# Performance work log

Hardware: AMD Instinct MI355X
Metric: run time of the kernel (lower is better)

The kernel has to match this reference:

```python
import jax, jax.numpy as jnp
import numpy as np

H, C = 4, 32            # heads, per-head out channels
N, E = 25000, 400000    # nodes, edges
NODE_DIM, EDGE_DIM = 256, 64
HC = H * C
IN_DIMS = [NODE_DIM, NODE_DIM + HC, NODE_DIM + HC]


def _conv(h, src, dst, ea, Wq, bq, Wk, bk, Wv, bv, We, Ws, bs):
    """One PyG-style TransformerConv (concat=True, root_weight=True, beta=False)."""
    n = h.shape[0]
    q = (h @ Wq + bq).reshape(n, H, C)
    k = (h @ Wk + bk).reshape(n, H, C)
    v = (h @ Wv + bv).reshape(n, H, C)
    e = (ea @ We).reshape(-1, H, C)            # lin_edge has no bias in PyG
    kj = k[src] + e                             # (E,H,C) key + edge feature
    alpha = jnp.einsum('ehc,ehc->eh', q[dst], kj) / jnp.asarray(np.sqrt(C), h.dtype)
    # segment softmax over incoming edges of each destination node
    amax = jax.ops.segment_max(alpha, dst, num_segments=n)
    ex = jnp.exp(alpha - amax[dst])
    denom = jax.ops.segment_sum(ex, dst, num_segments=n)
    a = ex / (denom[dst] + 1e-16)
    msg = (v[src] + e) * a[:, :, None]          # (E,H,C)
    out = jax.ops.segment_sum(msg, dst, num_segments=n).reshape(n, HC)
    return out + h @ Ws + bs                    # root/skip connection


def setup_inputs() -> dict:
    key = jax.random.key(0)
    ks = iter(jax.random.split(key, 64))
    inp = {}
    inp['x'] = jax.random.normal(next(ks), (N, NODE_DIM), dtype=jnp.float32)
    inp['edge_index'] = jax.random.randint(next(ks), (2, E), 0, N, dtype=jnp.int64)
    inp['edge_attr'] = jax.random.normal(next(ks), (E, EDGE_DIM), dtype=jnp.float32)
    s = 0.05
    for i, din in enumerate(IN_DIMS):
        inp[f'Wq{i}'] = jax.random.normal(next(ks), (din, HC), dtype=jnp.float32) * s
        inp[f'bq{i}'] = jnp.zeros((HC,), jnp.float32)
        inp[f'Wk{i}'] = jax.random.normal(next(ks), (din, HC), dtype=jnp.float32) * s
        inp[f'bk{i}'] = jnp.zeros((HC,), jnp.float32)
        inp[f'Wv{i}'] = jax.random.normal(next(ks), (din, HC), dtype=jnp.float32) * s
        inp[f'bv{i}'] = jnp.zeros((HC,), jnp.float32)
        inp[f'We{i}'] = jax.random.normal(next(ks), (EDGE_DIM, HC), dtype=jnp.float32) * s
        inp[f'Ws{i}'] = jax.random.normal(next(ks), (din, HC), dtype=jnp.float32) * s
        inp[f'bs{i}'] = jnp.zeros((HC,), jnp.float32)
    inp['Wout'] = jax.random.normal(next(ks), (HC, C), dtype=jnp.float32) * s
    inp['bout'] = jnp.zeros((C,), jnp.float32)
    return inp


def reference(x, edge_index, edge_attr,
              Wq0, bq0, Wk0, bk0, Wv0, bv0, We0, Ws0, bs0,
              Wq1, bq1, Wk1, bk1, Wv1, bv1, We1, Ws1, bs1,
              Wq2, bq2, Wk2, bk2, Wv2, bv2, We2, Ws2, bs2,
              Wout, bout):
    src, dst = edge_index[0], edge_index[1]
    params = [
        (Wq0, bq0, Wk0, bk0, Wv0, bv0, We0, Ws0, bs0),
        (Wq1, bq1, Wk1, bk1, Wv1, bv1, We1, Ws1, bs1),
        (Wq2, bq2, Wk2, bk2, Wv2, bv2, We2, Ws2, bs2),
    ]
    h = _conv(x, src, dst, edge_attr, *params[0])
    for p in params[1:]:
        h = _conv(jnp.concatenate([h, x], axis=-1), src, dst, edge_attr, *p)
    return h @ Wout + bout  # (N, output_dim)
```

## Files before the change

kernel.cpp:

```cpp
#include <hip/hip_runtime.h>
#include <hip/hip_bf16.h>
#include <math.h>

#define HCX 128
#define EDX 64
#define KPAD 384

typedef short bf16x8 __attribute__((ext_vector_type(8)));
typedef float f32x4  __attribute__((ext_vector_type(4)));

__device__ __forceinline__ short f2bf(float v) {
    __hip_bfloat16 b = __float2bfloat16(v);
    return *reinterpret_cast<short*>(&b);
}
__device__ __forceinline__ float bf2f(short s) {
    __hip_bfloat16 b = *reinterpret_cast<__hip_bfloat16*>(&s);
    return __bfloat162float(b);
}
__device__ __forceinline__ void gload16(const short* g, short* l) {
    __builtin_amdgcn_global_load_lds((const __attribute__((address_space(1))) void*)g,
                                     (__attribute__((address_space(3))) void*)l, 16, 0, 0);
}

__global__ __launch_bounds__(256) void k_zero_deg(int* __restrict__ deg, int n) {
    int t = blockIdx.x * 256 + threadIdx.x;
    if (t < n) deg[t] = 0;
}

__global__ __launch_bounds__(256) void k_hist(const int* __restrict__ dst, int* __restrict__ deg, int nE) {
    int t = blockIdx.x * 256 + threadIdx.x;
    if (t < nE) atomicAdd(&deg[dst[t]], 1);
}

__global__ __launch_bounds__(1024) void k_scan(const int* __restrict__ deg, int* __restrict__ csr_off,
                                               int* __restrict__ cursor, int nN) {
    __shared__ int sums[1024];
    int t = threadIdx.x;
    int chunk = (nN + 1023) >> 10;
    int lo = min(t * chunk, nN), hi = min(lo + chunk, nN);
    int s = 0;
    for (int i = lo; i < hi; ++i) s += deg[i];
    sums[t] = s;
    __syncthreads();
    for (int off = 1; off < 1024; off <<= 1) {
        int v = (t >= off) ? sums[t - off] : 0;
        __syncthreads();
        sums[t] += v;
        __syncthreads();
    }
    int run = (t == 0) ? 0 : sums[t - 1];
    for (int i = lo; i < hi; ++i) {
        csr_off[i] = run; cursor[i] = run;
        run += deg[i];
    }
    if (t == 1023) csr_off[nN] = sums[1023];
}

__global__ __launch_bounds__(256) void k_scatter(const int* __restrict__ dst, const int* __restrict__ src,
                                                 int* __restrict__ cursor,
                                                 int* __restrict__ edge_sorted, int* __restrict__ src_sorted,
                                                 int nE) {
    int t = blockIdx.x * 256 + threadIdx.x;
    if (t < nE) {
        int pos = atomicAdd(&cursor[dst[t]], 1);
        edge_sorted[pos] = t;
        src_sorted[pos]  = src[t];
    }
}

__global__ __launch_bounds__(256) void k_cvt_h(const float* __restrict__ pH, int has_h,
                                               short* __restrict__ Ah, short* __restrict__ Al,
                                               int nN, int Mpad)
{
    int t = blockIdx.x * 256 + threadIdx.x;
    int row = t >> 5;
    if (row >= Mpad) return;
    int c0 = (t & 31) * 4;
    float4 v = make_float4(0.f, 0.f, 0.f, 0.f);
    if (has_h && row < nN) v = *(const float4*)(pH + (size_t)row * HCX + c0);
    short4 hs, ls;
    hs.x = f2bf(v.x); ls.x = f2bf(v.x - bf2f(hs.x));
    hs.y = f2bf(v.y); ls.y = f2bf(v.y - bf2f(hs.y));
    hs.z = f2bf(v.z); ls.z = f2bf(v.z - bf2f(hs.z));
    hs.w = f2bf(v.w); ls.w = f2bf(v.w - bf2f(hs.w));
    *(short4*)(Ah + (size_t)row * KPAD + c0) = hs;
    *(short4*)(Al + (size_t)row * KPAD + c0) = ls;
}

__global__ __launch_bounds__(256) void k_cvt_x(const float* __restrict__ x,
                                               short* __restrict__ Ah, short* __restrict__ Al,
                                               int nN, int Mpad)
{
    int t = blockIdx.x * 256 + threadIdx.x;
    int row = t >> 6;
    if (row >= Mpad) return;
    int c0 = (t & 63) * 4;
    float4 v = make_float4(0.f, 0.f, 0.f, 0.f);
    if (row < nN) v = *(const float4*)(x + (size_t)row * 256 + c0);
    short4 hs, ls;
    hs.x = f2bf(v.x); ls.x = f2bf(v.x - bf2f(hs.x));
    hs.y = f2bf(v.y); ls.y = f2bf(v.y - bf2f(hs.y));
    hs.z = f2bf(v.z); ls.z = f2bf(v.z - bf2f(hs.z));
    hs.w = f2bf(v.w); ls.w = f2bf(v.w - bf2f(hs.w));
    *(short4*)(Ah + (size_t)row * KPAD + 128 + c0) = hs;
    *(short4*)(Al + (size_t)row * KPAD + 128 + c0) = ls;
}

__global__ __launch_bounds__(384) void k_cvt_W(const float* __restrict__ Wq, const float* __restrict__ Wk,
                                               const float* __restrict__ Wv, const float* __restrict__ Ws,
                                               int koff, int dinW,
                                               short* __restrict__ Wth, short* __restrict__ Wtl)
{
    int col = blockIdx.x;
    int g = col >> 7, c = col & 127;
    const float* W = (g == 0) ? Wq : (g == 1) ? Wk : (g == 2) ? Wv : Ws;
    for (int k = threadIdx.x; k < KPAD; k += blockDim.x) {
        int kr = k - koff;
        float v = (kr >= 0 && kr < dinW) ? W[(size_t)kr * HCX + c] : 0.f;
        short h = f2bf(v);
        Wth[(size_t)col * KPAD + k] = h;
        Wtl[(size_t)col * KPAD + k] = f2bf(v - bf2f(h));
    }
}

__global__ __launch_bounds__(256) void k_gemm(
    const short* __restrict__ Ah, const short* __restrict__ Al,
    const short* __restrict__ Wth, const short* __restrict__ Wtl,
    const float* __restrict__ bq, const float* __restrict__ bk,
    const float* __restrict__ bv, const float* __restrict__ bs,
    float* __restrict__ qkvs, int nN)
{
    __shared__ short AsH[128 * 32];
    __shared__ short AsL[128 * 32];
    __shared__ short BsH[128 * 32];
    __shared__ short BsL[128 * 32];

    const int rowB = blockIdx.x * 128;
    const int g = blockIdx.y;
    const int colB = g * 128;
    const int tid = threadIdx.x;
    const int w = tid >> 6, l = tid & 63;

    f32x4 acc[4][4];
    #pragma unroll
    for (int i = 0; i < 4; ++i)
        #pragma unroll
        for (int j = 0; j < 4; ++j)
            acc[i][j] = (f32x4){0.f, 0.f, 0.f, 0.f};

    const int lrow4 = l >> 2;
    const int gch = (l & 3) ^ ((l >> 3) & 3);
    const int lr = l & 15, kg = l >> 4;

    for (int ks = 0; ks < KPAD / 32; ++ks) {
        const int k0 = ks * 32;
        #pragma unroll
        for (int jj = 0; jj < 2; ++jj) {
            int j = w + jj * 4;
            int rr = j * 16 + lrow4;
            size_t aoff = (size_t)(rowB + rr) * KPAD + k0 + gch * 8;
            size_t boff = (size_t)(colB + rr) * KPAD + k0 + gch * 8;
            gload16(Ah  + aoff, AsH + j * 512);
            gload16(Al  + aoff, AsL + j * 512);
            gload16(Wth + boff, BsH + j * 512);
            gload16(Wtl + boff, BsL + j * 512);
        }
        __syncthreads();

        bf16x8 ah[4], am[4], bh[4], bm[4];
        #pragma unroll
        for (int mi = 0; mi < 4; ++mi) {
            int r = (w >> 1) * 64 + mi * 16 + lr;
            int ch = kg ^ ((r >> 1) & 3);
            int off = r * 32 + ch * 8;
            ah[mi] = *(const bf16x8*)(AsH + off);
            am[mi] = *(const bf16x8*)(AsL + off);
        }
        #pragma unroll
        for (int ni = 0; ni < 4; ++ni) {
            int c = (w & 1) * 64 + ni * 16 + lr;
            int ch = kg ^ ((c >> 1) & 3);
            int off = c * 32 + ch * 8;
            bh[ni] = *(const bf16x8*)(BsH + off);
            bm[ni] = *(const bf16x8*)(BsL + off);
        }
        #pragma unroll
        for (int mi = 0; mi < 4; ++mi)
            #pragma unroll
            for (int ni = 0; ni < 4; ++ni) {
                acc[mi][ni] = __builtin_amdgcn_mfma_f32_16x16x32_bf16(ah[mi], bh[ni], acc[mi][ni], 0, 0, 0);
                acc[mi][ni] = __builtin_amdgcn_mfma_f32_16x16x32_bf16(ah[mi], bm[ni], acc[mi][ni], 0, 0, 0);
                acc[mi][ni] = __builtin_amdgcn_mfma_f32_16x16x32_bf16(am[mi], bh[ni], acc[mi][ni], 0, 0, 0);
            }
        __syncthreads();
    }

    const float* bias = (g == 0) ? bq : (g == 1) ? bk : (g == 2) ? bv : bs;
    float* outp = qkvs + (size_t)g * nN * HCX;
    const int lq = l >> 4;
    #pragma unroll
    for (int mi = 0; mi < 4; ++mi)
        #pragma unroll
        for (int ni = 0; ni < 4; ++ni) {
            int c = (w & 1) * 64 + ni * 16 + lr;
            float bb = bias[c];
            #pragma unroll
            for (int j = 0; j < 4; ++j) {
                int r = rowB + (w >> 1) * 64 + mi * 16 + lq * 4 + j;
                if (r < nN) outp[(size_t)r * HCX + c] = acc[mi][ni][j] + bb;
            }
        }
}

__global__ __launch_bounds__(256) void k_qwe(const float* __restrict__ qpl,
                                             const float* __restrict__ We,
                                             float* __restrict__ qWe, int nN)
{
    __shared__ float Wes[64 * 128];
    __shared__ float qs[16][128];
    for (int i = threadIdx.x; i < 64 * 128; i += 256) {
        int d = i >> 7, c = i & 127;
        Wes[d * 128 + ((c + d) & 127)] = We[i];
    }
    int nb = blockIdx.x * 16;
    for (int i = threadIdx.x; i < 16 * 128; i += 256) {
        int r = i >> 7, c = i & 127;
        int row = nb + r;
        qs[r][c] = (row < nN) ? qpl[(size_t)row * HCX + c] : 0.f;
    }
    __syncthreads();
    int h = threadIdx.x >> 6, d = threadIdx.x & 63;
    const int base = h * 32;
    for (int r = 0; r < 16; ++r) {
        int row = nb + r;
        if (row >= nN) break;
        float s = 0.f;
        #pragma unroll
        for (int c = 0; c < 32; ++c)
            s += qs[r][base + c] * Wes[d * 128 + ((base + c + d) & 127)];
        qWe[(size_t)row * 256 + threadIdx.x] = s;
    }
}

__global__ __launch_bounds__(256) void k_edge(
    const float* __restrict__ qkvs, const float* __restrict__ qWe,
    const float* __restrict__ ea,   const float* __restrict__ We,
    const int* __restrict__ csr_off, const int* __restrict__ edge_sorted,
    const int* __restrict__ src_sorted,
    float* __restrict__ hout, int nN)
{
    __shared__ float wea_s[4][4][64];
    const int wv = threadIdx.x >> 6, l = threadIdx.x & 63;
    const int n = blockIdx.x * 4 + wv;
    const bool active = n < nN;
    int o0 = 0, o1 = 0;
    if (active) { o0 = csr_off[n]; o1 = csr_off[n + 1]; }

    const float* qpl = qkvs;
    const float* kpl = qkvs + (size_t)nN * HCX;
    const float* vpl = qkvs + 2 * (size_t)nN * HCX;

    float qr0 = 0.f, qr1 = 0.f, qw0 = 0.f, qw1 = 0.f, qw2 = 0.f, qw3 = 0.f;
    if (active) {
        qr0 = qpl[(size_t)n * HCX + l];
        qr1 = qpl[(size_t)n * HCX + 64 + l];
        const float* qw = qWe + (size_t)n * 256;
        qw0 = qw[l]; qw1 = qw[64 + l]; qw2 = qw[128 + l]; qw3 = qw[192 + l];
    }
    const int hsel = l >> 5;
    const float scale = 0.17677669529663687f;

    float m0 = -INFINITY, m1 = -INFINITY, m2 = -INFINITY, m3 = -INFINITY;
    float den0 = 0.f, den1 = 0.f, den2 = 0.f, den3 = 0.f;
    float w0 = 0.f, w1 = 0.f, w2 = 0.f, w3 = 0.f;
    float macc0 = 0.f, macc1 = 0.f;

    for (int i = o0; i < o1; ++i) {
        int eid = edge_sorted[i];
        int sn  = src_sorted[i];
        float kv0 = kpl[(size_t)sn * HCX + l];
        float kv1 = kpl[(size_t)sn * HCX + 64 + l];
        float vv0 = vpl[(size_t)sn * HCX + l];
        float vv1 = vpl[(size_t)sn * HCX + 64 + l];
        float eav = ea[(size_t)eid * EDX + l];

        float p1 = qr0 * kv0, p2 = qr1 * kv1;
        #pragma unroll
        for (int s = 1; s < 32; s <<= 1) {
            p1 += __shfl_xor(p1, s);
            p2 += __shfl_xor(p2, s);
        }
        float p1o = __shfl_xor(p1, 32), p2o = __shfl_xor(p2, 32);
        float qk0 = hsel ? p1o : p1, qk1 = hsel ? p1 : p1o;
        float qk2 = hsel ? p2o : p2, qk3 = hsel ? p2 : p2o;

        float t0 = eav * qw0, t1 = eav * qw1, t2 = eav * qw2, t3 = eav * qw3;
        #pragma unroll
        for (int s = 1; s < 64; s <<= 1) {
            t0 += __shfl_xor(t0, s); t1 += __shfl_xor(t1, s);
            t2 += __shfl_xor(t2, s); t3 += __shfl_xor(t3, s);
        }

        float s0 = (qk0 + t0) * scale, s1 = (qk1 + t1) * scale;
        float s2 = (qk2 + t2) * scale, s3 = (qk3 + t3) * scale;

        float nm0 = fmaxf(m0, s0), nm1 = fmaxf(m1, s1);
        float nm2 = fmaxf(m2, s2), nm3 = fmaxf(m3, s3);
        float f0 = __expf(m0 - nm0), f1 = __expf(m1 - nm1);
        float f2 = __expf(m2 - nm2), f3 = __expf(m3 - nm3);
        float e0 = __expf(s0 - nm0), e1 = __expf(s1 - nm1);
        float e2 = __expf(s2 - nm2), e3 = __expf(s3 - nm3);
        m0 = nm0; m1 = nm1; m2 = nm2; m3 = nm3;
        den0 = den0 * f0 + e0; den1 = den1 * f1 + e1;
        den2 = den2 * f2 + e2; den3 = den3 * f3 + e3;
        w0 = w0 * f0 + e0 * eav; w1 = w1 * f1 + e1 * eav;
        w2 = w2 * f2 + e2 * eav; w3 = w3 * f3 + e3 * eav;
        float fA = hsel ? f1 : f0, eA = hsel ? e1 : e0;
        float fB = hsel ? f3 : f2, eB = hsel ? e3 : e2;
        macc0 = macc0 * fA + eA * vv0;
        macc1 = macc1 * fB + eB * vv1;
    }

    wea_s[wv][0][l] = w0; wea_s[wv][1][l] = w1;
    wea_s[wv][2][l] = w2; wea_s[wv][3][l] = w3;
    __syncthreads();

    float acc1 = macc0, acc2 = macc1;
    const int h1 = hsel, h2 = 2 + hsel;
    #pragma unroll 8
    for (int d = 0; d < 64; ++d) {
        acc1 += wea_s[wv][h1][d] * We[d * HCX + l];
        acc2 += wea_s[wv][h2][d] * We[d * HCX + 64 + l];
    }
    if (active) {
        float d1 = (hsel ? den1 : den0) + 1e-16f;
        float d2 = (hsel ? den3 : den2) + 1e-16f;
        const float* spl = qkvs + 3 * (size_t)nN * HCX + (size_t)n * HCX;
        hout[(size_t)n * HCX + l]      = acc1 / d1 + spl[l];
        hout[(size_t)n * HCX + 64 + l] = acc2 / d2 + spl[64 + l];
    }
}

__global__ __launch_bounds__(256) void k_out(const float* __restrict__ h,
                                             const float* __restrict__ Wout,
                                             const float* __restrict__ bout,
                                             float* __restrict__ out, int nN)
{
    __shared__ float hs[8][128];
    int nb = blockIdx.x * 8;
    for (int i = threadIdx.x; i < 8 * 128; i += 256) {
        int r = i >> 7, c = i & 127;
        int row = nb + r;
        hs[r][c] = (row < nN) ? h[(size_t)row * 128 + c] : 0.f;
    }
    __syncthreads();
    int r = threadIdx.x >> 5, col = threadIdx.x & 31;
    int row = nb + r;
    if (row < nN) {
        float s = bout[col];
        #pragma unroll 16
        for (int c = 0; c < 128; ++c) s += hs[r][c] * Wout[c * 32 + col];
        out[(size_t)row * 32 + col] = s;
    }
}

static inline size_t align_up(size_t v, size_t a) { return (v + a - 1) & ~(a - 1); }

extern "C" void kernel_launch(void* const* d_in, const int* in_sizes, int n_in,
                              void* d_out, int out_size, void* d_ws, size_t ws_size,
                              hipStream_t stream)
{
    const float* x  = (const float*)d_in[0];
    const int*   ei = (const int*)d_in[1];
    const float* ea = (const float*)d_in[2];
    const int nN = in_sizes[0] / 256;
    const int nE = in_sizes[1] / 2;
    const int Mpad = (nN + 127) & ~127;
    const int* src = ei;
    const int* dst = ei + nE;

    char* p = (char*)d_ws;
    size_t off = 0;
    auto take = [&](size_t bytes) { void* r = p + off; off = align_up(off + bytes, 256); return r; };
    int* csr_off     = (int*)take((size_t)(nN + 1) * 4);
    int* cursor      = (int*)take((size_t)nN * 4);
    int* deg         = (int*)take((size_t)nN * 4);
    int* edge_sorted = (int*)take((size_t)nE * 4);
    int* src_sorted  = (int*)take((size_t)nE * 4);
    float* qkvs = (float*)take((size_t)4 * nN * HCX * 4);
    float* qWe  = (float*)take((size_t)nN * 256 * 4);
    float* h0   = (float*)take((size_t)nN * HCX * 4);
    float* h1   = (float*)take((size_t)nN * HCX * 4);
    short* Ah   = (short*)take((size_t)Mpad * KPAD * 2);
    short* Al   = (short*)take((size_t)Mpad * KPAD * 2);
    short* Wth  = (short*)take((size_t)512 * KPAD * 2);
    short* Wtl  = (short*)take((size_t)512 * KPAD * 2);
    (void)ws_size; (void)n_in; (void)out_size;

    k_zero_deg<<<(nN + 255) / 256, 256, 0, stream>>>(deg, nN);
    k_hist<<<(nE + 255) / 256, 256, 0, stream>>>(dst, deg, nE);
    k_scan<<<1, 1024, 0, stream>>>(deg, csr_off, cursor, nN);
    k_scatter<<<(nE + 255) / 256, 256, 0, stream>>>(dst, src, cursor, edge_sorted, src_sorted, nE);

    k_cvt_x<<<(Mpad * 64 + 255) / 256, 256, 0, stream>>>(x, Ah, Al, nN, Mpad);

    auto layer = [&](const float* pH, int has_h, int base, float* hout) {
        const float* Wq = (const float*)d_in[base + 0];
        const float* bq = (const float*)d_in[base + 1];
        const float* Wk = (const float*)d_in[base + 2];
        const float* bk = (const float*)d_in[base + 3];
        const float* Wv = (const float*)d_in[base + 4];
        const float* bv = (const float*)d_in[base + 5];
        const float* We = (const float*)d_in[base + 6];
        const float* Ws = (const float*)d_in[base + 7];
        const float* bs = (const float*)d_in[base + 8];
        int koff = has_h ? 0 : 128;
        int dinW = has_h ? 384 : 256;
        k_cvt_h<<<(Mpad * 32 + 255) / 256, 256, 0, stream>>>(pH, has_h, Ah, Al, nN, Mpad);
        k_cvt_W<<<512, 384, 0, stream>>>(Wq, Wk, Wv, Ws, koff, dinW, Wth, Wtl);
        dim3 gg(Mpad / 128, 4);
        k_gemm<<<gg, 256, 0, stream>>>(Ah, Al, Wth, Wtl, bq, bk, bv, bs, qkvs, nN);
        k_qwe<<<(nN + 15) / 16, 256, 0, stream>>>(qkvs, We, qWe, nN);
        k_edge<<<(nN + 3) / 4, 256, 0, stream>>>(qkvs, qWe, ea, We,
                                                 csr_off, edge_sorted, src_sorted, hout, nN);
    };

    layer(nullptr, 0, 3,  h0);
    layer(h0, 1,   12, h1);
    layer(h1, 1,   21, h0);

    k_out<<<(nN + 7) / 8, 256, 0, stream>>>(h0, (const float*)d_in[30], (const float*)d_in[31],
                                            (float*)d_out, nN);
}
```

Measured before the change: 1.130 ms.

## Split edge attention into per-edge score kernel and per-node aggregation

Moves the attention score computation into a separate edge-parallel kernel that writes exp(score) per edge and head, so the per-node aggregation loop no longer does shuffle reductions or online-softmax rescaling. A dst_sorted array is added so each edge thread can find its destination's query. The max subtraction is dropped, so exp can overflow for large scores, and the extra expA buffer adds global memory traffic.

Measured after the change: 1.134 ms. No clear change (+0.4%).

```diff
diff --git a/kernel.cpp b/kernel.cpp
--- a/kernel.cpp
+++ b/kernel.cpp
@@ -59,12 +59,14 @@
 __global__ __launch_bounds__(256) void k_scatter(const int* __restrict__ dst, const int* __restrict__ src,
                                                  int* __restrict__ cursor,
                                                  int* __restrict__ edge_sorted, int* __restrict__ src_sorted,
-                                                 int nE) {
+                                                 int* __restrict__ dst_sorted, int nE) {
     int t = blockIdx.x * 256 + threadIdx.x;
     if (t < nE) {
-        int pos = atomicAdd(&cursor[dst[t]], 1);
+        int d = dst[t];
+        int pos = atomicAdd(&cursor[d], 1);
         edge_sorted[pos] = t;
         src_sorted[pos]  = src[t];
+        dst_sorted[pos]  = d;
     }
 }
 
@@ -242,8 +244,41 @@
     }
 }
 
-__global__ __launch_bounds__(256) void k_edge(
+__global__ __launch_bounds__(256) void k_alpha(
     const float* __restrict__ qkvs, const float* __restrict__ qWe,
+    const float* __restrict__ ea,
+    const int* __restrict__ edge_sorted, const int* __restrict__ src_sorted,
+    const int* __restrict__ dst_sorted,
+    float* __restrict__ expA, int nN, int nE)
+{
+    int t = blockIdx.x * 256 + threadIdx.x;
+    int i = t >> 2, h = t & 3;
+    if (i >= nE) return;
+    int sn = src_sorted[i], dn = dst_sorted[i];
+    int eid = edge_sorted[i];
+
+    const float* q = qkvs + (size_t)dn * HCX + h * 32;
+    const float* k = qkvs + (size_t)nN * HCX + (size_t)sn * HCX + h * 32;
+    float s = 0.f;
+    #pragma unroll
+    for (int c = 0; c < 32; c += 4) {
+        float4 qv = *(const float4*)(q + c);
+        float4 kv = *(const float4*)(k + c);
+        s += qv.x * kv.x + qv.y * kv.y + qv.z * kv.z + qv.w * kv.w;
+    }
+    const float* qw = qWe + (size_t)dn * 256 + h * 64;
+    const float* ev = ea + (size_t)eid * EDX;
+    #pragma unroll
+    for (int d = 0; d < EDX; d += 4) {
+        float4 av = *(const float4*)(ev + d);
+        float4 wv = *(const float4*)(qw + d);
+        s += av.x * wv.x + av.y * wv.y + av.z * wv.z + av.w * wv.w;
+    }
+    expA[t] = __expf(s * 0.17677669529663687f);
+}
+
+__global__ __launch_bounds__(256) void k_edge2(
+    const float* __restrict__ qkvs, const float* __restrict__ expA,
     const float* __restrict__ ea,   const float* __restrict__ We,
     const int* __restrict__ csr_off, const int* __restrict__ edge_sorted,
     const int* __restrict__ src_sorted,
@@ -256,69 +291,28 @@
     int o0 = 0, o1 = 0;
     if (active) { o0 = csr_off[n]; o1 = csr_off[n + 1]; }
 
-    const float* qpl = qkvs;
-    const float* kpl = qkvs + (size_t)nN * HCX;
     const float* vpl = qkvs + 2 * (size_t)nN * HCX;
-
-    float qr0 = 0.f, qr1 = 0.f, qw0 = 0.f, qw1 = 0.f, qw2 = 0.f, qw3 = 0.f;
-    if (active) {
-        qr0 = qpl[(size_t)n * HCX + l];
-        qr1 = qpl[(size_t)n * HCX + 64 + l];
-        const float* qw = qWe + (size_t)n * 256;
-        qw0 = qw[l]; qw1 = qw[64 + l]; qw2 = qw[128 + l]; qw3 = qw[192 + l];
-    }
     const int hsel = l >> 5;
-    const float scale = 0.17677669529663687f;
-
-    float m0 = -INFINITY, m1 = -INFINITY, m2 = -INFINITY, m3 = -INFINITY;
+
     float den0 = 0.f, den1 = 0.f, den2 = 0.f, den3 = 0.f;
     float w0 = 0.f, w1 = 0.f, w2 = 0.f, w3 = 0.f;
     float macc0 = 0.f, macc1 = 0.f;
 
+    #pragma unroll 2
     for (int i = o0; i < o1; ++i) {
+        float4 e4 = *(const float4*)(expA + (size_t)i * 4);
         int eid = edge_sorted[i];
         int sn  = src_sorted[i];
-        float kv0 = kpl[(size_t)sn * HCX + l];
-        float kv1 = kpl[(size_t)sn * HCX + 64 + l];
+        float eav = ea[(size_t)eid * EDX + l];
         float vv0 = vpl[(size_t)sn * HCX + l];
         float vv1 = vpl[(size_t)sn * HCX + 64 + l];
-        float eav = ea[(size_t)eid * EDX + l];
-
-        float p1 = qr0 * kv0, p2 = qr1 * kv1;
-        #pragma unroll
-        for (int s = 1; s < 32; s <<= 1) {
-            p1 += __shfl_xor(p1, s);
-            p2 += __shfl_xor(p2, s);
-        }
-        float p1o = __shfl_xor(p1, 32), p2o = __shfl_xor(p2, 32);
-        float qk0 = hsel ? p1o : p1, qk1 = hsel ? p1 : p1o;
-        float qk2 = hsel ? p2o : p2, qk3 = hsel ? p2 : p2o;
-
-        float t0 = eav * qw0, t1 = eav * qw1, t2 = eav * qw2, t3 = eav * qw3;
-        #pragma unroll
-        for (int s = 1; s < 64; s <<= 1) {
-            t0 += __shfl_xor(t0, s); t1 += __shfl_xor(t1, s);
-            t2 += __shfl_xor(t2, s); t3 += __shfl_xor(t3, s);
-        }
-
-        float s0 = (qk0 + t0) * scale, s1 = (qk1 + t1) * scale;
-        float s2 = (qk2 + t2) * scale, s3 = (qk3 + t3) * scale;
-
-        float nm0 = fmaxf(m0, s0), nm1 = fmaxf(m1, s1);
-        float nm2 = fmaxf(m2, s2), nm3 = fmaxf(m3, s3);
-        float f0 = __expf(m0 - nm0), f1 = __expf(m1 - nm1);
-        float f2 = __expf(m2 - nm2), f3 = __expf(m3 - nm3);
-        float e0 = __expf(s0 - nm0), e1 = __expf(s1 - nm1);
-        float e2 = __expf(s2 - nm2), e3 = __expf(s3 - nm3);
-        m0 = nm0; m1 = nm1; m2 = nm2; m3 = nm3;
-        den0 = den0 * f0 + e0; den1 = den1 * f1 + e1;
-        den2 = den2 * f2 + e2; den3 = den3 * f3 + e3;
-        w0 = w0 * f0 + e0 * eav; w1 = w1 * f1 + e1 * eav;
-        w2 = w2 * f2 + e2 * eav; w3 = w3 * f3 + e3 * eav;
-        float fA = hsel ? f1 : f0, eA = hsel ? e1 : e0;
-        float fB = hsel ? f3 : f2, eB = hsel ? e3 : e2;
-        macc0 = macc0 * fA + eA * vv0;
-        macc1 = macc1 * fB + eB * vv1;
+
+        den0 += e4.x; den1 += e4.y; den2 += e4.z; den3 += e4.w;
+        w0 += e4.x * eav; w1 += e4.y * eav; w2 += e4.z * eav; w3 += e4.w * eav;
+        float eA = hsel ? e4.y : e4.x;
+        float eB = hsel ? e4.w : e4.z;
+        macc0 += eA * vv0;
+        macc1 += eB * vv1;
     }
 
     wea_s[wv][0][l] = w0; wea_s[wv][1][l] = w1;
@@ -387,8 +381,10 @@
     int* deg         = (int*)take((size_t)nN * 4);
     int* edge_sorted = (int*)take((size_t)nE * 4);
     int* src_sorted  = (int*)take((size_t)nE * 4);
+    int* dst_sorted  = (int*)take((size_t)nE * 4);
     float* qkvs = (float*)take((size_t)4 * nN * HCX * 4);
     float* qWe  = (float*)take((size_t)nN * 256 * 4);
+    float* expA = (float*)take((size_t)nE * 4 * 4);
     float* h0   = (float*)take((size_t)nN * HCX * 4);
     float* h1   = (float*)take((size_t)nN * HCX * 4);
     short* Ah   = (short*)take((size_t)Mpad * KPAD * 2);
@@ -400,7 +396,8 @@
     k_zero_deg<<<(nN + 255) / 256, 256, 0, stream>>>(deg, nN);
     k_hist<<<(nE + 255) / 256, 256, 0, stream>>>(dst, deg, nE);
     k_scan<<<1, 1024, 0, stream>>>(deg, csr_off, cursor, nN);
-    k_scatter<<<(nE + 255) / 256, 256, 0, stream>>>(dst, src, cursor, edge_sorted, src_sorted, nE);
+    k_scatter<<<(nE + 255) / 256, 256, 0, stream>>>(dst, src, cursor,
+                                                    edge_sorted, src_sorted, dst_sorted, nE);
 
     k_cvt_x<<<(Mpad * 64 + 255) / 256, 256, 0, stream>>>(x, Ah, Al, nN, Mpad);
 
@@ -421,8 +418,11 @@
         dim3 gg(Mpad / 128, 4);
         k_gemm<<<gg, 256, 0, stream>>>(Ah, Al, Wth, Wtl, bq, bk, bv, bs, qkvs, nN);
         k_qwe<<<(nN + 15) / 16, 256, 0, stream>>>(qkvs, We, qWe, nN);
-        k_edge<<<(nN + 3) / 4, 256, 0, stream>>>(qkvs, qWe, ea, We,
-                                                 csr_off, edge_sorted, src_sorted, hout, nN);
+        k_alpha<<<(nE * 4 + 255) / 256, 256, 0, stream>>>(qkvs, qWe, ea,
+                                                          edge_sorted, src_sorted, dst_sorted,
+                                                          expA, nN, nE);
+        k_edge2<<<(nN + 3) / 4, 256, 0, stream>>>(qkvs, expA, ea, We,
+                                                  csr_off, edge_sorted, src_sorted, hout, nN);
     };
 
     layer(nullptr, 0, 3,  h0);
```
